# Optimization experiments

Measured on AMD Instinct MI355X. Metric: run time of the kernel, lower is better.

The kernel has to match this reference:

```python
import jax, jax.numpy as jnp
import numpy as np

N, T, D, H = 32, 4096, 256, 512  # n_mlps, tokens per mlp, d_model, hidden


def setup_inputs() -> dict:
    key = jax.random.key(0)
    k_x, k_w1, k_w2 = jax.random.split(key, 3)
    x = jax.random.normal(k_x, (N, T, D), dtype=jnp.float32)
    # per-MLP weights stacked along the expert dim; init ~ torch Linear default scale
    W1 = jax.random.normal(k_w1, (N, H, D), dtype=jnp.float32) / np.sqrt(D)
    b1 = jnp.zeros((N, H), dtype=jnp.float32)
    W2 = jax.random.normal(k_w2, (N, D, H), dtype=jnp.float32) / np.sqrt(H)
    b2 = jnp.zeros((N, D), dtype=jnp.float32)
    return {"x": x, "W1": W1, "b1": b1, "W2": W2, "b2": b2}


def reference(x, W1, b1, W2, b2):
    # outputs[i] = mlp_i(x[i]); stack + residual add.
    # Expressed as a single grouped (batched) GEMM over the expert dim n.
    h = jnp.einsum('ntd,nhd->nth', x, W1) + b1[:, None, :]   # [N,T,H]
    h = jax.nn.silu(h)
    out = jnp.einsum('nth,ndh->ntd', h, W2) + b2[:, None, :]  # [N,T,D]
    return out + x
```

## Files before the change

kernel.cpp:

```cpp
#include <hip/hip_runtime.h>
#include <hip/hip_bf16.h>


#define N_EXP 32
#define T_TOK 4096
#define D_MOD 256
#define H_HID 512

#define BT 64
#define HC 32
#define NCHUNK 16
#define NTHREADS 256

#define NWELEM 4194304ull
#define WS_NEEDED (8ull * NWELEM)

typedef __attribute__((ext_vector_type(8))) __bf16 bf16x8;
typedef __attribute__((ext_vector_type(4))) __bf16 bf16x4;
typedef __attribute__((ext_vector_type(4))) float  f32x4;
union U4 { uint4 q; bf16x8 v; };

static __device__ __forceinline__ f32x4 mfma16(bf16x8 a, bf16x8 b, f32x4 c) {
  return __builtin_amdgcn_mfma_f32_16x16x32_bf16(a, b, c, 0, 0, 0);
}

static __device__ __forceinline__ void split8(const float v[8], bf16x8& hi, bf16x8& lo) {
#pragma unroll
  for (int j = 0; j < 8; ++j) {
    float f = v[j];
    __bf16 h = (__bf16)f;
    hi[j] = h;
    lo[j] = (__bf16)(f - (float)h);
  }
}

static __device__ __forceinline__ void gl_lds16(const __bf16* g, __bf16* l) {
  __builtin_amdgcn_global_load_lds(
      (const __attribute__((address_space(1))) void*)g,
      (__attribute__((address_space(3))) void*)l, 16, 0, 0);
}

#define BAR_LGKM() do { asm volatile("s_waitcnt lgkmcnt(0)" ::: "memory"); \
  __builtin_amdgcn_s_barrier(); __builtin_amdgcn_sched_barrier(0); } while (0)
#define BAR_VM(n) do { asm volatile("s_waitcnt vmcnt(" #n ")" ::: "memory"); \
  __builtin_amdgcn_s_barrier(); __builtin_amdgcn_sched_barrier(0); } while (0)

__global__ __launch_bounds__(256)
void presplit_w(const float* __restrict__ W1, const float* __restrict__ W2,
                __bf16* __restrict__ ws) {
  unsigned U = blockIdx.x * 256 + threadIdx.x;
  {
    unsigned row = U >> 5;
    unsigned u   = U & 31;
    const float* src = W1 + ((size_t)U << 3);
    float4 a0 = *(const float4*)src, a1 = *(const float4*)(src + 4);
    float v[8] = {a0.x, a0.y, a0.z, a0.w, a1.x, a1.y, a1.z, a1.w};
    bf16x8 hi, lo; split8(v, hi, lo);
    size_t dst = (((size_t)row << 5) | (u ^ (row & 7))) << 3;
    *(bf16x8*)(ws + dst)          = hi;
    *(bf16x8*)(ws + NWELEM + dst) = lo;
  }
  {
    unsigned r = U >> 6;
    unsigned e = r >> 8, d = r & 255;
    unsigned u = U & 63;
    unsigned c = u >> 2, uc = u & 3;
    const float* src = W2 + ((size_t)U << 3);
    float4 a0 = *(const float4*)src, a1 = *(const float4*)(src + 4);
    float v[8] = {a0.x, a0.y, a0.z, a0.w, a1.x, a1.y, a1.z, a1.w};
    bf16x8 hi, lo; split8(v, hi, lo);
    size_t dst = (((((size_t)((e << 4) + c) << 8) + d) << 2) | (uc ^ ((d >> 1) & 3))) << 3;
    *(bf16x8*)(ws + 2 * NWELEM + dst) = hi;
    *(bf16x8*)(ws + 3 * NWELEM + dst) = lo;
  }
}

__global__ __launch_bounds__(NTHREADS, 2)
void pmlp_fused(const float* __restrict__ x, const float* __restrict__ b1g,
                const float* __restrict__ b2g, float* __restrict__ out,
                const __bf16* __restrict__ wsp) {
  __shared__ __bf16 W1h[HC * D_MOD],   W1l[HC * D_MOD];
  __shared__ __bf16 W2h[D_MOD * HC],   W2l[D_MOD * HC];
  __shared__ unsigned APK[BT * 32];
  __shared__ float b1s[H_HID];

  const int tid = threadIdx.x;

  const int p    = blockIdx.x;
  const int xcd  = p & 7;
  const int slot = p >> 3;
  const int e    = xcd + ((slot >> 6) << 3);
  const int ti   = slot & 63;

  const float* xb = x + ((size_t)e * T_TOK + (size_t)ti * BT) * D_MOD;
  float*       ob = out + ((size_t)e * T_TOK + (size_t)ti * BT) * D_MOD;

  const int l    = tid & 63;
  const int w    = tid >> 6;
  const int lrow = l & 15;
  const int lk8  = (l >> 4) << 3;
  const int lr4  = (l >> 4) << 2;
  const int g1_r = (w & 1) << 5;
  const int g1_c = (w >> 1) << 4;

  b1s[tid]       = b1g[e * H_HID + tid];
  b1s[tid + 256] = b1g[e * H_HID + tid + 256];

  bf16x8 xh[2][8], xl[2][8];
#pragma unroll
  for (int mf = 0; mf < 2; ++mf)
#pragma unroll
    for (int kk = 0; kk < 8; ++kk) {
      const float* s = xb + (g1_r + (mf << 4) + lrow) * D_MOD + (kk << 5) + lk8;
      float4 u0 = *(const float4*)s;
      float4 u1 = *(const float4*)(s + 4);
      float v[8] = {u0.x, u0.y, u0.z, u0.w, u1.x, u1.y, u1.z, u1.w};
      split8(v, xh[mf][kk], xl[mf][kk]);
    }

  const __bf16* w1h_img = wsp;
  const __bf16* w1l_img = wsp + NWELEM;
  const __bf16* w2h_img = wsp + 2 * NWELEM;
  const __bf16* w2l_img = wsp + 3 * NWELEM;

  auto stageW1 = [&](int c) {
    size_t gb = ((size_t)(e * NCHUNK + c)) << 13;
#pragma unroll
    for (int s = 0; s < 4; ++s) {
      int off = ((w << 2) + s) << 9;
      int go  = off + (l << 3);
      gl_lds16(w1h_img + gb + go, &W1h[off]);
      gl_lds16(w1l_img + gb + go, &W1l[off]);
    }
  };
  auto stageW2 = [&](int c) {
    size_t gb = ((size_t)(e * NCHUNK + c)) << 13;
#pragma unroll
    for (int s = 0; s < 4; ++s) {
      int off = ((w << 2) + s) << 9;
      int go  = off + (l << 3);
      gl_lds16(w2h_img + gb + go, &W2h[off]);
      gl_lds16(w2l_img + gb + go, &W2l[off]);
    }
  };

  const f32x4 fz = {0.f, 0.f, 0.f, 0.f};
  f32x4 acc2[4][4];
#pragma unroll
  for (int mf = 0; mf < 4; ++mf)
#pragma unroll
    for (int nf = 0; nf < 4; ++nf) acc2[mf][nf] = fz;

  asm volatile("" ::: "memory");
  stageW1(0);
  stageW2(0);
  asm volatile("s_waitcnt vmcnt(8)\n\ts_waitcnt lgkmcnt(0)" ::: "memory");
  __builtin_amdgcn_s_barrier();
  __builtin_amdgcn_sched_barrier(0);

  for (int c = 0; c < NCHUNK; ++c) {
    f32x4 acc1[2] = {fz, fz};
    const int r1 = g1_c + lrow;
#pragma unroll
    for (int kk = 0; kk < 8; ++kk) {
      int uu = (((kk << 2) + (lk8 >> 3)) ^ (r1 & 7)) << 3;
      bf16x8 bh = *(const bf16x8*)&W1h[(r1 << 8) + uu];
      bf16x8 bl = *(const bf16x8*)&W1l[(r1 << 8) + uu];
#pragma unroll
      for (int mf = 0; mf < 2; ++mf) {
        acc1[mf] = mfma16(xh[mf][kk], bh, acc1[mf]);
        acc1[mf] = mfma16(xh[mf][kk], bl, acc1[mf]);
        acc1[mf] = mfma16(xl[mf][kk], bh, acc1[mf]);
      }
    }
    float b1v = b1s[c * HC + g1_c + lrow];
    int acol = g1_c + lrow;
#pragma unroll
    for (int mf = 0; mf < 2; ++mf)
#pragma unroll
      for (int r = 0; r < 4; ++r) {
        float hv = acc1[mf][r] + b1v;
        hv = hv / (1.f + __expf(-hv));
        __bf16 hh = (__bf16)hv;
        __bf16 hl = (__bf16)(hv - (float)hh);
        unsigned pk = (unsigned)__builtin_bit_cast(unsigned short, hh) |
                      ((unsigned)__builtin_bit_cast(unsigned short, hl) << 16);
        int arow = g1_r + (mf << 4) + lr4 + r;
        APK[arow * 32 + ((((acol >> 2) ^ (arow & 7)) << 2) | (acol & 3))] = pk;
      }
    BAR_LGKM();

    if (c < NCHUNK - 1) {
      stageW1(c + 1);
      BAR_VM(8);
    } else {
      BAR_VM(0);
    }

    bf16x8 bh2[4], bl2[4];
#pragma unroll
    for (int nf = 0; nf < 4; ++nf) {
      int dcol = (w << 6) + (nf << 4) + lrow;
      int up = (((lk8 >> 3) ^ ((dcol >> 1) & 3)) << 3);
      bh2[nf] = *(const bf16x8*)&W2h[(dcol << 5) + up];
      bl2[nf] = *(const bf16x8*)&W2l[(dcol << 5) + up];
    }
#pragma unroll
    for (int mf = 0; mf < 4; ++mf) {
      int m  = (mf << 4) + lrow;
      int u1 = lk8 >> 2;
      uint4 qa = *(const uint4*)&APK[m * 32 + ((u1 ^ (m & 7)) << 2)];
      uint4 qb = *(const uint4*)&APK[m * 32 + (((u1 + 1) ^ (m & 7)) << 2)];
      U4 ah, al;
      ah.q.x = (qa.x & 0xFFFFu) | (qa.y << 16);
      ah.q.y = (qa.z & 0xFFFFu) | (qa.w << 16);
      ah.q.z = (qb.x & 0xFFFFu) | (qb.y << 16);
      ah.q.w = (qb.z & 0xFFFFu) | (qb.w << 16);
      al.q.x = (qa.x >> 16) | (qa.y & 0xFFFF0000u);
      al.q.y = (qa.z >> 16) | (qa.w & 0xFFFF0000u);
      al.q.z = (qb.x >> 16) | (qb.y & 0xFFFF0000u);
      al.q.w = (qb.z >> 16) | (qb.w & 0xFFFF0000u);
#pragma unroll
      for (int nf = 0; nf < 4; ++nf) {
        acc2[mf][nf] = mfma16(ah.v, bh2[nf], acc2[mf][nf]);
        acc2[mf][nf] = mfma16(ah.v, bl2[nf], acc2[mf][nf]);
        acc2[mf][nf] = mfma16(al.v, bh2[nf], acc2[mf][nf]);
      }
    }
    BAR_LGKM();

    if (c < NCHUNK - 1) {
      stageW2(c + 1);
      BAR_VM(8);
    }
  }

#pragma unroll
  for (int mf = 0; mf < 4; ++mf)
#pragma unroll
    for (int r = 0; r < 4; ++r) {
      int trow = (mf << 4) + lr4 + r;
#pragma unroll
      for (int nf = 0; nf < 4; ++nf) {
        int dcol = (w << 6) + (nf << 4) + lrow;
        ob[trow * D_MOD + dcol] = acc2[mf][nf][r] + b2g[e * D_MOD + dcol]
                                + xb[trow * D_MOD + dcol];
      }
    }
}

#define WPITCH 264
__global__ __launch_bounds__(NTHREADS, 2)
void pmlp_fb(const float* __restrict__ x, const float* __restrict__ W1,
             const float* __restrict__ b1, const float* __restrict__ W2,
             const float* __restrict__ b2, float* __restrict__ out) {
  __shared__ __bf16 W1h[HC * WPITCH], W1l[HC * WPITCH];
  __shared__ __bf16 W2h[D_MOD * 32],  W2l[D_MOD * 32];
  __shared__ unsigned APK[BT * 32];

  const int tid = threadIdx.x;
  const int p = blockIdx.x, xcd = p & 7, slot = p >> 3;
  const int e = xcd + ((slot >> 6) << 3), ti = slot & 63;
  const float* xb = x + ((size_t)e * T_TOK + (size_t)ti * BT) * D_MOD;
  float*       ob = out + ((size_t)e * T_TOK + (size_t)ti * BT) * D_MOD;
  const int l = tid & 63, w = tid >> 6;
  const int lrow = l & 15, lk8 = (l >> 4) << 3, lr4 = (l >> 4) << 2;
  const int g1_r = (w & 1) << 5, g1_c = (w >> 1) << 4;

  bf16x8 xh[2][8], xl[2][8];
#pragma unroll
  for (int mf = 0; mf < 2; ++mf)
#pragma unroll
    for (int kk = 0; kk < 8; ++kk) {
      const float* s = xb + (g1_r + (mf << 4) + lrow) * D_MOD + (kk << 5) + lk8;
      float4 u0 = *(const float4*)s, u1 = *(const float4*)(s + 4);
      float v[8] = {u0.x, u0.y, u0.z, u0.w, u1.x, u1.y, u1.z, u1.w};
      split8(v, xh[mf][kk], xl[mf][kk]);
    }

  float s1[4][8], s2[4][8];
  auto loadW = [&](int c) {
#pragma unroll
    for (int k2 = 0; k2 < 4; ++k2) {
      int g = tid + (k2 << 8);
      int r1 = g >> 5, c1 = (g & 31) << 3;
      int r2 = g >> 2, c2 = (g & 3) << 3;
      const float* sp1 = W1 + ((size_t)e * H_HID + c * HC + r1) * D_MOD + c1;
      const float* sp2 = W2 + ((size_t)e * D_MOD + r2) * H_HID + c * HC + c2;
      float4 u0 = *(const float4*)sp1, u1 = *(const float4*)(sp1 + 4);
      s1[k2][0]=u0.x; s1[k2][1]=u0.y; s1[k2][2]=u0.z; s1[k2][3]=u0.w;
      s1[k2][4]=u1.x; s1[k2][5]=u1.y; s1[k2][6]=u1.z; s1[k2][7]=u1.w;
      float4 v0 = *(const float4*)sp2, v1 = *(const float4*)(sp2 + 4);
      s2[k2][0]=v0.x; s2[k2][1]=v0.y; s2[k2][2]=v0.z; s2[k2][3]=v0.w;
      s2[k2][4]=v1.x; s2[k2][5]=v1.y; s2[k2][6]=v1.z; s2[k2][7]=v1.w;
    }
  };
  auto writeW = [&]() {
#pragma unroll
    for (int k2 = 0; k2 < 4; ++k2) {
      int g = tid + (k2 << 8);
      int r1 = g >> 5, c1 = (g & 31) << 3;
      int r2 = g >> 2, u2 = g & 3;
      int sw2 = ((u2 ^ (r2 & 3)) << 3);
      bf16x8 hi, lo;
      split8(s1[k2], hi, lo);
      *(bf16x8*)&W1h[r1 * WPITCH + c1] = hi;
      *(bf16x8*)&W1l[r1 * WPITCH + c1] = lo;
      split8(s2[k2], hi, lo);
      *(bf16x8*)&W2h[r2 * 32 + sw2] = hi;
      *(bf16x8*)&W2l[r2 * 32 + sw2] = lo;
    }
  };

  const f32x4 fz = {0.f, 0.f, 0.f, 0.f};
  f32x4 acc2[4][4];
#pragma unroll
  for (int mf = 0; mf < 4; ++mf)
#pragma unroll
    for (int nf = 0; nf < 4; ++nf) acc2[mf][nf] = fz;

  loadW(0); writeW();
  __syncthreads();

  for (int c = 0; c < NCHUNK; ++c) {
    if (c < NCHUNK - 1) loadW(c + 1);
    float b1v = b1[e * H_HID + c * HC + g1_c + lrow];
    f32x4 acc1[2] = {fz, fz};
#pragma unroll
    for (int kk = 0; kk < 8; ++kk) {
      int k = (kk << 5) + lk8;
      bf16x8 bh = *(const bf16x8*)&W1h[(g1_c + lrow) * WPITCH + k];
      bf16x8 bl = *(const bf16x8*)&W1l[(g1_c + lrow) * WPITCH + k];
#pragma unroll
      for (int mf = 0; mf < 2; ++mf) {
        acc1[mf] = mfma16(xh[mf][kk], bh, acc1[mf]);
        acc1[mf] = mfma16(xh[mf][kk], bl, acc1[mf]);
        acc1[mf] = mfma16(xl[mf][kk], bh, acc1[mf]);
      }
    }
    int acol = g1_c + lrow;
#pragma unroll
    for (int mf = 0; mf < 2; ++mf)
#pragma unroll
      for (int r = 0; r < 4; ++r) {
        float hv = acc1[mf][r] + b1v;
        hv = hv / (1.f + __expf(-hv));
        __bf16 hh = (__bf16)hv;
        __bf16 hl = (__bf16)(hv - (float)hh);
        unsigned pk = (unsigned)__builtin_bit_cast(unsigned short, hh) |
                      ((unsigned)__builtin_bit_cast(unsigned short, hl) << 16);
        int arow = g1_r + (mf << 4) + lr4 + r;
        APK[arow * 32 + ((((acol >> 2) ^ (arow & 7)) << 2) | (acol & 3))] = pk;
      }
    __syncthreads();

    bf16x8 bh2[4], bl2[4];
#pragma unroll
    for (int nf = 0; nf < 4; ++nf) {
      int dcol = (w << 6) + (nf << 4) + lrow;
      int sw = (((lk8 >> 3) ^ (dcol & 3)) << 3);
      bh2[nf] = *(const bf16x8*)&W2h[dcol * 32 + sw];
      bl2[nf] = *(const bf16x8*)&W2l[dcol * 32 + sw];
    }
#pragma unroll
    for (int mf = 0; mf < 4; ++mf) {
      int m = (mf << 4) + lrow, u1 = lk8 >> 2;
      uint4 qa = *(const uint4*)&APK[m * 32 + ((u1 ^ (m & 7)) << 2)];
      uint4 qb = *(const uint4*)&APK[m * 32 + (((u1 + 1) ^ (m & 7)) << 2)];
      U4 ah, al;
      ah.q.x = (qa.x & 0xFFFFu) | (qa.y << 16);
      ah.q.y = (qa.z & 0xFFFFu) | (qa.w << 16);
      ah.q.z = (qb.x & 0xFFFFu) | (qb.y << 16);
      ah.q.w = (qb.z & 0xFFFFu) | (qb.w << 16);
      al.q.x = (qa.x >> 16) | (qa.y & 0xFFFF0000u);
      al.q.y = (qa.z >> 16) | (qa.w & 0xFFFF0000u);
      al.q.z = (qb.x >> 16) | (qb.y & 0xFFFF0000u);
      al.q.w = (qb.z >> 16) | (qb.w & 0xFFFF0000u);
#pragma unroll
      for (int nf = 0; nf < 4; ++nf) {
        acc2[mf][nf] = mfma16(ah.v, bh2[nf], acc2[mf][nf]);
        acc2[mf][nf] = mfma16(ah.v, bl2[nf], acc2[mf][nf]);
        acc2[mf][nf] = mfma16(al.v, bh2[nf], acc2[mf][nf]);
      }
    }
    __syncthreads();
    if (c < NCHUNK - 1) { writeW(); __syncthreads(); }
  }

#pragma unroll
  for (int mf = 0; mf < 4; ++mf)
#pragma unroll
    for (int r = 0; r < 4; ++r) {
      int trow = (mf << 4) + lr4 + r;
#pragma unroll
      for (int nf = 0; nf < 4; ++nf) {
        int dcol = (w << 6) + (nf << 4) + lrow;
        ob[trow * D_MOD + dcol] = acc2[mf][nf][r] + b2[e * D_MOD + dcol]
                                + xb[trow * D_MOD + dcol];
      }
    }
}

extern "C" void kernel_launch(void* const* d_in, const int* in_sizes, int n_in,
                              void* d_out, int out_size, void* d_ws, size_t ws_size,
                              hipStream_t stream) {
  const float* x  = (const float*)d_in[0];
  const float* W1 = (const float*)d_in[1];
  const float* b1 = (const float*)d_in[2];
  const float* W2 = (const float*)d_in[3];
  const float* b2 = (const float*)d_in[4];
  float* out = (float*)d_out;
  __bf16* ws = (__bf16*)d_ws;

  dim3 grid(N_EXP * (T_TOK / BT));
  dim3 block(NTHREADS);

  if (ws_size >= WS_NEEDED) {
    hipLaunchKernelGGL(presplit_w, dim3(2048), dim3(256), 0, stream, W1, W2, ws);
    hipLaunchKernelGGL(pmlp_fused, grid, block, 0, stream,
                       x, b1, b2, out, (const __bf16*)ws);
  } else {
    hipLaunchKernelGGL(pmlp_fb, grid, block, 0, stream, x, W1, b1, W2, b2, out);
  }
}
```

Before: 494.0 us.

## Remap GEMM1 warps to 16-row token strips and raise MFMA wave priority

Each of the four waves now owns 16 token rows and all 32 hidden columns of a chunk in the first GEMM, where before each owned 32 rows and 16 columns. This halves the x fragments held in registers (8 hi/lo bf16x8 pairs instead of 16), freeing VGPRs that may help occupancy or scheduling. The cost is reading twice as many W1 fragments from LDS per chunk. s_setprio is also raised around the MFMA loops of both GEMMs so the MFMA-issuing waves get precedence over the other waves.

```diff
diff --git a/kernel.cpp b/kernel.cpp
--- a/kernel.cpp
+++ b/kernel.cpp
@@ -100,23 +100,20 @@
   const int lrow = l & 15;
   const int lk8  = (l >> 4) << 3;
   const int lr4  = (l >> 4) << 2;
-  const int g1_r = (w & 1) << 5;
-  const int g1_c = (w >> 1) << 4;
+  const int g1_r = w << 4;
 
   b1s[tid]       = b1g[e * H_HID + tid];
   b1s[tid + 256] = b1g[e * H_HID + tid + 256];
 
-  bf16x8 xh[2][8], xl[2][8];
-#pragma unroll
-  for (int mf = 0; mf < 2; ++mf)
-#pragma unroll
-    for (int kk = 0; kk < 8; ++kk) {
-      const float* s = xb + (g1_r + (mf << 4) + lrow) * D_MOD + (kk << 5) + lk8;
-      float4 u0 = *(const float4*)s;
-      float4 u1 = *(const float4*)(s + 4);
-      float v[8] = {u0.x, u0.y, u0.z, u0.w, u1.x, u1.y, u1.z, u1.w};
-      split8(v, xh[mf][kk], xl[mf][kk]);
-    }
+  bf16x8 xh[8], xl[8];
+#pragma unroll
+  for (int kk = 0; kk < 8; ++kk) {
+    const float* s = xb + (g1_r + lrow) * D_MOD + (kk << 5) + lk8;
+    float4 u0 = *(const float4*)s;
+    float4 u1 = *(const float4*)(s + 4);
+    float v[8] = {u0.x, u0.y, u0.z, u0.w, u1.x, u1.y, u1.z, u1.w};
+    split8(v, xh[kk], xl[kk]);
+  }
 
   const __bf16* w1h_img = wsp;
   const __bf16* w1l_img = wsp + NWELEM;
@@ -160,34 +157,37 @@
 
   for (int c = 0; c < NCHUNK; ++c) {
     f32x4 acc1[2] = {fz, fz};
-    const int r1 = g1_c + lrow;
+    __builtin_amdgcn_s_setprio(1);
 #pragma unroll
     for (int kk = 0; kk < 8; ++kk) {
-      int uu = (((kk << 2) + (lk8 >> 3)) ^ (r1 & 7)) << 3;
-      bf16x8 bh = *(const bf16x8*)&W1h[(r1 << 8) + uu];
-      bf16x8 bl = *(const bf16x8*)&W1l[(r1 << 8) + uu];
-#pragma unroll
-      for (int mf = 0; mf < 2; ++mf) {
-        acc1[mf] = mfma16(xh[mf][kk], bh, acc1[mf]);
-        acc1[mf] = mfma16(xh[mf][kk], bl, acc1[mf]);
-        acc1[mf] = mfma16(xl[mf][kk], bh, acc1[mf]);
-      }
-    }
-    float b1v = b1s[c * HC + g1_c + lrow];
-    int acol = g1_c + lrow;
-#pragma unroll
-    for (int mf = 0; mf < 2; ++mf)
+#pragma unroll
+      for (int cf = 0; cf < 2; ++cf) {
+        int r1 = (cf << 4) + lrow;
+        int uu = (((kk << 2) + (lk8 >> 3)) ^ (r1 & 7)) << 3;
+        bf16x8 bh = *(const bf16x8*)&W1h[(r1 << 8) + uu];
+        bf16x8 bl = *(const bf16x8*)&W1l[(r1 << 8) + uu];
+        acc1[cf] = mfma16(xh[kk], bh, acc1[cf]);
+        acc1[cf] = mfma16(xh[kk], bl, acc1[cf]);
+        acc1[cf] = mfma16(xl[kk], bh, acc1[cf]);
+      }
+    }
+    __builtin_amdgcn_s_setprio(0);
+#pragma unroll
+    for (int cf = 0; cf < 2; ++cf) {
+      int acol = (cf << 4) + lrow;
+      float b1v = b1s[c * HC + acol];
 #pragma unroll
       for (int r = 0; r < 4; ++r) {
-        float hv = acc1[mf][r] + b1v;
+        float hv = acc1[cf][r] + b1v;
         hv = hv / (1.f + __expf(-hv));
         __bf16 hh = (__bf16)hv;
         __bf16 hl = (__bf16)(hv - (float)hh);
         unsigned pk = (unsigned)__builtin_bit_cast(unsigned short, hh) |
                       ((unsigned)__builtin_bit_cast(unsigned short, hl) << 16);
-        int arow = g1_r + (mf << 4) + lr4 + r;
+        int arow = g1_r + lr4 + r;
         APK[arow * 32 + ((((acol >> 2) ^ (arow & 7)) << 2) | (acol & 3))] = pk;
       }
+    }
     BAR_LGKM();
 
     if (c < NCHUNK - 1) {
@@ -220,12 +220,14 @@
       al.q.y = (qa.z >> 16) | (qa.w & 0xFFFF0000u);
       al.q.z = (qb.x >> 16) | (qb.y & 0xFFFF0000u);
       al.q.w = (qb.z >> 16) | (qb.w & 0xFFFF0000u);
+      __builtin_amdgcn_s_setprio(1);
 #pragma unroll
       for (int nf = 0; nf < 4; ++nf) {
         acc2[mf][nf] = mfma16(ah.v, bh2[nf], acc2[mf][nf]);
         acc2[mf][nf] = mfma16(ah.v, bl2[nf], acc2[mf][nf]);
         acc2[mf][nf] = mfma16(al.v, bh2[nf], acc2[mf][nf]);
       }
+      __builtin_amdgcn_s_setprio(0);
     }
     BAR_LGKM();
 
@@ -265,18 +267,16 @@
   float*       ob = out + ((size_t)e * T_TOK + (size_t)ti * BT) * D_MOD;
   const int l = tid & 63, w = tid >> 6;
   const int lrow = l & 15, lk8 = (l >> 4) << 3, lr4 = (l >> 4) << 2;
-  const int g1_r = (w & 1) << 5, g1_c = (w >> 1) << 4;
-
-  bf16x8 xh[2][8], xl[2][8];
-#pragma unroll
-  for (int mf = 0; mf < 2; ++mf)
-#pragma unroll
-    for (int kk = 0; kk < 8; ++kk) {
-      const float* s = xb + (g1_r + (mf << 4) + lrow) * D_MOD + (kk << 5) + lk8;
-      float4 u0 = *(const float4*)s, u1 = *(const float4*)(s + 4);
-      float v[8] = {u0.x, u0.y, u0.z, u0.w, u1.x, u1.y, u1.z, u1.w};
-      split8(v, xh[mf][kk], xl[mf][kk]);
-    }
+  const int g1_r = w << 4;
+
+  bf16x8 xh[8], xl[8];
+#pragma unroll
+  for (int kk = 0; kk < 8; ++kk) {
+    const float* s = xb + (g1_r + lrow) * D_MOD + (kk << 5) + lk8;
+    float4 u0 = *(const float4*)s, u1 = *(const float4*)(s + 4);
+    float v[8] = {u0.x, u0.y, u0.z, u0.w, u1.x, u1.y, u1.z, u1.w};
+    split8(v, xh[kk], xl[kk]);
+  }
 
   float s1[4][8], s2[4][8];
   auto loadW = [&](int c) {
@@ -324,34 +324,36 @@
 
   for (int c = 0; c < NCHUNK; ++c) {
     if (c < NCHUNK - 1) loadW(c + 1);
-    float b1v = b1[e * H_HID + c * HC + g1_c + lrow];
     f32x4 acc1[2] = {fz, fz};
 #pragma unroll
     for (int kk = 0; kk < 8; ++kk) {
-      int k = (kk << 5) + lk8;
-      bf16x8 bh = *(const bf16x8*)&W1h[(g1_c + lrow) * WPITCH + k];
-      bf16x8 bl = *(const bf16x8*)&W1l[(g1_c + lrow) * WPITCH + k];
-#pragma unroll
-      for (int mf = 0; mf < 2; ++mf) {
-        acc1[mf] = mfma16(xh[mf][kk], bh, acc1[mf]);
-        acc1[mf] = mfma16(xh[mf][kk], bl, acc1[mf]);
-        acc1[mf] = mfma16(xl[mf][kk], bh, acc1[mf]);
-      }
-    }
-    int acol = g1_c + lrow;
-#pragma unroll
-    for (int mf = 0; mf < 2; ++mf)
+#pragma unroll
+      for (int cf = 0; cf < 2; ++cf) {
+        int r1 = (cf << 4) + lrow;
+        int k = (kk << 5) + lk8;
+        bf16x8 bh = *(const bf16x8*)&W1h[r1 * WPITCH + k];
+        bf16x8 bl = *(const bf16x8*)&W1l[r1 * WPITCH + k];
+        acc1[cf] = mfma16(xh[kk], bh, acc1[cf]);
+        acc1[cf] = mfma16(xh[kk], bl, acc1[cf]);
+        acc1[cf] = mfma16(xl[kk], bh, acc1[cf]);
+      }
+    }
+#pragma unroll
+    for (int cf = 0; cf < 2; ++cf) {
+      int acol = (cf << 4) + lrow;
+      float b1v = b1[e * H_HID + c * HC + acol];
 #pragma unroll
       for (int r = 0; r < 4; ++r) {
-        float hv = acc1[mf][r] + b1v;
+        float hv = acc1[cf][r] + b1v;
         hv = hv / (1.f + __expf(-hv));
         __bf16 hh = (__bf16)hv;
         __bf16 hl = (__bf16)(hv - (float)hh);
         unsigned pk = (unsigned)__builtin_bit_cast(unsigned short, hh) |
                       ((unsigned)__builtin_bit_cast(unsigned short, hl) << 16);
-        int arow = g1_r + (mf << 4) + lr4 + r;
+        int arow = g1_r + lr4 + r;
         APK[arow * 32 + ((((acol >> 2) ^ (arow & 7)) << 2) | (acol & 3))] = pk;
       }
+    }
     __syncthreads();
 
     bf16x8 bh2[4], bl2[4];
```

New measurement: 439.7 us. 1.12x faster.
